# Kernel tuning notes

Hardware: AMD Instinct MI355X
Metric: run time of the kernel (lower is better)

Reference implementation:

```python
import jax, jax.numpy as jnp
import numpy as np
import math

B, T, F_ = 4, 1024, 1024
TO_DIM, FROM_DIM, LATENT, H = 1024, 1024, 1024, 16
HEAD_DIM = LATENT // H

def _linear_params(key, in_dim, out_dim):
    kw, kb = jax.random.split(key)
    bound = 1.0 / math.sqrt(in_dim)
    W = jax.random.uniform(kw, (out_dim, in_dim), minval=-bound, maxval=bound, dtype=jnp.float32)
    b = jax.random.uniform(kb, (out_dim,), minval=-bound, maxval=bound, dtype=jnp.float32)
    return W, b

def setup_inputs() -> dict:
    key = jax.random.key(0)
    ks = jax.random.split(key, 7)
    X_to = jax.random.normal(ks[0], (B, T, TO_DIM), dtype=jnp.float32)
    X_from = jax.random.normal(ks[1], (B, F_, FROM_DIM), dtype=jnp.float32)
    mask_from = jax.random.randint(ks[2], (B, T, F_), 0, 2, dtype=jnp.int32)
    Wq, bq = _linear_params(ks[3], TO_DIM, LATENT)
    Wk, bk = _linear_params(ks[4], FROM_DIM, LATENT)
    Wv, bv = _linear_params(ks[5], FROM_DIM, LATENT)
    Wo, bo = _linear_params(ks[6], LATENT, TO_DIM)
    return {"X_to": X_to, "X_from": X_from, "mask_from": mask_from,
            "Wq": Wq, "bq": bq, "Wk": Wk, "bk": bk, "Wv": Wv, "bv": bv, "Wo": Wo, "bo": bo}

def _split_heads(x):
    # [b, t, (h k)] -> [b, h, t, k]
    b, t, _ = x.shape
    return x.reshape(b, t, H, HEAD_DIM).transpose(0, 2, 1, 3)

def reference(X_to, X_from, mask_from, Wq, bq, Wk, bk, Wv, bv, Wo, bo):
    Q = _split_heads(X_to @ Wq.T + bq)
    # NOTE: source swaps names — K comes from v_linear, V from k_linear. Reproduced literally.
    K = _split_heads(X_from @ Wv.T + bv)
    V = _split_heads(X_from @ Wk.T + bk)
    attn = jnp.einsum('bhtk,bhfk->bhtf', Q, K) / math.sqrt(HEAD_DIM)
    attn = jnp.where(mask_from[:, None, :, :] == 0, jnp.float32(-10000.0), attn)
    attn = jax.nn.softmax(attn, axis=-1)
    out = jnp.einsum('bhtf,bhfk->bhtk', attn, V)  # [b,h,t,k]
    out = out.transpose(0, 2, 1, 3).reshape(X_to.shape[0], X_to.shape[1], LATENT)
    return out @ Wo.T + bo
```

## Files before the change

### kernel.cpp

```cpp
#include <hip/hip_runtime.h>
#include <hip/hip_bf16.h>
#include <math.h>

#define BB 4
#define TT 1024
#define FF 1024
#define DIM 1024
#define NH 16
#define HD 64
#define MROWS (BB * TT)
#define FB (FF / 64)

typedef __attribute__((ext_vector_type(8))) short short8;
typedef __attribute__((ext_vector_type(4))) short short4v;
typedef __attribute__((ext_vector_type(4))) float f32x4;
typedef __hip_bfloat16 bf16;

__device__ __forceinline__ void async_copy16(const void* g, void* l) {
    __builtin_amdgcn_global_load_lds((const __attribute__((address_space(1))) void*)g,
                                     (__attribute__((address_space(3))) void*)l,
                                     16, 0, 0);
}

struct ConvArgs {
    const float* src[6];
    bf16* dst[6];
    int nvec[6];
    int blk_end[6];
    const int* mask;
    unsigned long long* Mb;
};

__global__ __launch_bounds__(256) void convert_pack(ConvArgs a) {
    int bx = blockIdx.x;
    if (bx >= a.blk_end[5]) {
        const int lane = threadIdx.x & 63;
        const int waveId = (bx - a.blk_end[5]) * 4 + (threadIdx.x >> 6);
#pragma unroll
        for (int it = 0; it < 16; ++it) {
            int c = waveId * 16 + it;
            int v = a.mask[(size_t)c * 64 + lane];
            unsigned long long bits = __ballot(v != 0);
            if (lane == 0) a.Mb[c] = bits;
        }
        return;
    }
    int seg = 0;
#pragma unroll
    for (int k = 0; k < 5; ++k) if (bx >= a.blk_end[k]) seg = k + 1;
    int b0 = seg ? a.blk_end[seg - 1] : 0;
    int idx = (bx - b0) * 256 + threadIdx.x;
    if (idx >= a.nvec[seg]) return;
    float4 v = ((const float4*)a.src[seg])[idx];
    union { bf16 t[4]; ushort4 u; } o;
    o.t[0] = __float2bfloat16(v.x);
    o.t[1] = __float2bfloat16(v.y);
    o.t[2] = __float2bfloat16(v.z);
    o.t[3] = __float2bfloat16(v.w);
    *(ushort4*)(a.dst[seg] + 4 * (size_t)idx) = o.u;
}

#define BK 64

struct QkvArgs {
    const bf16* A[3]; const bf16* W[3]; const float* bias[3]; bf16* C[3];
    int N[3]; int biasRow[3];
};

__global__ __launch_bounds__(256) void gemm_qkv(QkvArgs q) {
    __shared__ bf16 smem[128 * 132];
    bf16* As = smem;
    bf16* Bs = smem + 128 * BK;

    const int op = blockIdx.z;
    const bf16* A = q.A[op];
    const bf16* W = q.W[op];
    const float* bias = q.bias[op];
    bf16* C = q.C[op];
    const int N = q.N[op];
    const int brow = q.biasRow[op];

    const int lin = blockIdx.x + 8 * blockIdx.y;
    const int xcd = lin & 7;
    const int t   = lin >> 3;
    int m0, n0;
    if (brow) {
        m0 = (((t & 7) + xcd) & 7) * 128;
        n0 = (xcd * 4 + (t >> 3)) * 128;
    } else {
        m0 = (xcd * 4 + (t >> 3)) * 128;
        n0 = (((t & 7) + xcd) & 7) * 128;
    }

    const int tid  = threadIdx.x;
    const int lane = tid & 63;
    const int wave = tid >> 6;
    const int quad = lane >> 4;
    const int l16  = lane & 15;
    const int wm = wave & 1;
    const int wn = wave >> 1;
    const int wbase = tid & ~63;

    f32x4 acc[4][4] = {};

    for (int k0 = 0; k0 < DIM; k0 += BK) {
#pragma unroll
        for (int j = 0; j < 4; ++j) {
            int slot = j * 256 + tid;
            int r = slot >> 3;
            int g = (slot & 7) ^ (r & 7);
            async_copy16(A + (size_t)(m0 + r) * DIM + k0 + g * 8,
                         As + (size_t)(j * 256 + wbase) * 8);
            async_copy16(W + (size_t)(n0 + r) * DIM + k0 + g * 8,
                         Bs + (size_t)(j * 256 + wbase) * 8);
        }
        __syncthreads();

#pragma unroll
        for (int kk = 0; kk < 2; ++kk) {
            short8 a[4], b[4];
#pragma unroll
            for (int mi = 0; mi < 4; ++mi) {
                int r = wm * 64 + mi * 16 + l16;
                int p = (kk * 4 + quad) ^ (r & 7);
                a[mi] = *(const short8*)(As + r * BK + p * 8);
            }
#pragma unroll
            for (int ni = 0; ni < 4; ++ni) {
                int r = wn * 64 + ni * 16 + l16;
                int p = (kk * 4 + quad) ^ (r & 7);
                b[ni] = *(const short8*)(Bs + r * BK + p * 8);
            }
#pragma unroll
            for (int mi = 0; mi < 4; ++mi)
#pragma unroll
                for (int ni = 0; ni < 4; ++ni)
                    acc[mi][ni] = __builtin_amdgcn_mfma_f32_16x16x32_bf16(
                        a[mi], b[ni], acc[mi][ni], 0, 0, 0);
        }
        __syncthreads();
    }

    bf16* Cs = smem;
#pragma unroll
    for (int ni = 0; ni < 4; ++ni) {
        const int nl = wn * 64 + ni * 16 + l16;
        float bcol = brow ? 0.0f : bias[n0 + nl];
#pragma unroll
        for (int mi = 0; mi < 4; ++mi)
#pragma unroll
            for (int i = 0; i < 4; ++i) {
                const int ml = wm * 64 + mi * 16 + quad * 4 + i;
                float v = acc[mi][ni][i] + (brow ? bias[m0 + ml] : bcol);
                Cs[ml * 132 + nl] = __float2bfloat16(v);
            }
    }
    __syncthreads();
#pragma unroll
    for (int j = 0; j < 8; ++j) {
        int slot = j * 256 + tid;
        int rr = slot >> 4, cc = slot & 15;
        short8 v = *(const short8*)(Cs + rr * 132 + cc * 8);
        *(short8*)(C + (size_t)(m0 + rr) * N + n0 + cc * 8) = v;
    }
}

__global__ __launch_bounds__(256) void gemm_o(
    const bf16* __restrict__ A, const bf16* __restrict__ W,
    const float* __restrict__ bias, float* __restrict__ C)
{
    __shared__ float smemf[128 * 66];
    bf16* As = (bf16*)smemf;
    bf16* Bs = As + 128 * BK;

    const int lin = blockIdx.x + 16 * blockIdx.y;
    const int xcd = lin & 7;
    const int t   = lin >> 3;
    const int m0 = (xcd * 4 + (t >> 4)) * 128;
    const int n0 = (((t & 15) + 2 * xcd) & 15) * 64;

    const int tid  = threadIdx.x;
    const int lane = tid & 63;
    const int wave = tid >> 6;
    const int quad = lane >> 4;
    const int l16  = lane & 15;
    const int wm = wave & 1;
    const int wn = wave >> 1;
    const int wbase = tid & ~63;

    f32x4 acc[4][2] = {};

    for (int k0 = 0; k0 < DIM; k0 += BK) {
#pragma unroll
        for (int j = 0; j < 4; ++j) {
            int slot = j * 256 + tid;
            int r = slot >> 3;
            int g = (slot & 7) ^ (r & 7);
            async_copy16(A + (size_t)(m0 + r) * DIM + k0 + g * 8,
                         As + (size_t)(j * 256 + wbase) * 8);
        }
#pragma unroll
        for (int j = 0; j < 2; ++j) {
            int slot = j * 256 + tid;
            int r = slot >> 3;
            int g = (slot & 7) ^ (r & 7);
            async_copy16(W + (size_t)(n0 + r) * DIM + k0 + g * 8,
                         Bs + (size_t)(j * 256 + wbase) * 8);
        }
        __syncthreads();

#pragma unroll
        for (int kk = 0; kk < 2; ++kk) {
            short8 a[4], b[2];
#pragma unroll
            for (int mi = 0; mi < 4; ++mi) {
                int r = wm * 64 + mi * 16 + l16;
                int p = (kk * 4 + quad) ^ (r & 7);
                a[mi] = *(const short8*)(As + r * BK + p * 8);
            }
#pragma unroll
            for (int ni = 0; ni < 2; ++ni) {
                int r = wn * 32 + ni * 16 + l16;
                int p = (kk * 4 + quad) ^ (r & 7);
                b[ni] = *(const short8*)(Bs + r * BK + p * 8);
            }
#pragma unroll
            for (int mi = 0; mi < 4; ++mi)
#pragma unroll
                for (int ni = 0; ni < 2; ++ni)
                    acc[mi][ni] = __builtin_amdgcn_mfma_f32_16x16x32_bf16(
                        a[mi], b[ni], acc[mi][ni], 0, 0, 0);
        }
        __syncthreads();
    }

    float* Cs = smemf;
#pragma unroll
    for (int ni = 0; ni < 2; ++ni) {
        const int nl = wn * 32 + ni * 16 + l16;
        const float bcol = bias[n0 + nl];
#pragma unroll
        for (int mi = 0; mi < 4; ++mi)
#pragma unroll
            for (int i = 0; i < 4; ++i) {
                const int ml = wm * 64 + mi * 16 + quad * 4 + i;
                Cs[ml * 66 + nl] = acc[mi][ni][i] + bcol;
            }
    }
    __syncthreads();
#pragma unroll
    for (int j = 0; j < 8; ++j) {
        int slot = j * 256 + tid;
        int rr = slot >> 4, cc = slot & 15;
        float4 v = *(const float4*)(Cs + rr * 66 + cc * 4);
        *(float4*)(C + (size_t)(m0 + rr) * DIM + n0 + cc * 4) = v;
    }
}

__global__ __launch_bounds__(256, 4) void attn_kernel(
    const bf16* Qg, const bf16* __restrict__ Kg, const bf16* __restrict__ Vtg,
    const unsigned long long* __restrict__ Mbits, bf16* Og)
{
    __shared__ bf16 Ks[128 * 64];
    __shared__ bf16 Vts[64 * 128];
    __shared__ bf16 Pt[64 * 136];
    __shared__ float ls[64];

    const int tid  = threadIdx.x;
    const int lane = tid & 63;
    const int wave = tid >> 6;
    const int quad = lane >> 4;
    const int l16  = lane & 15;

    const int lin = blockIdx.x + 16 * (blockIdx.y + 16 * blockIdx.z);
    const int xcd = lin & 7;
    const int t   = lin >> 3;
    const int bh  = xcd * 8 + (t >> 4);
    const int b   = bh >> 4;
    const int h   = bh & 15;
    const int t0  = (t & 15) * 64;

    const size_t qrow0 = (size_t)b * TT + t0;
    const size_t krow0 = (size_t)b * FF;
    const int wbase = tid & ~63;
    const int myrow = wave * 16 + l16;

    const bf16* qptr = Qg + (qrow0 + myrow) * DIM + h * HD;
    short8 qb0 = *(const short8*)(qptr + quad * 8);
    short8 qb1 = *(const short8*)(qptr + 32 + quad * 8);

    const unsigned long long* mrow = Mbits + (qrow0 + myrow) * FB;
    unsigned long long w0 = mrow[0];
    unsigned long long w1 = mrow[1];

    float lsum = 0.f;
    f32x4 oacc[4] = {};

#pragma unroll 1
    for (int it = 0; it < 8; ++it) {
        const int f0 = it * 128;
#pragma unroll
        for (int j = 0; j < 4; ++j) {
            int slot = j * 256 + tid;
            int rk = slot >> 3;
            int gk = (slot & 7) ^ (rk & 7);
            async_copy16(Kg + (krow0 + f0 + rk) * DIM + h * HD + gk * 8,
                         Ks + (size_t)(j * 256 + wbase) * 8);
            int rv = slot >> 4;
            int gv = (slot & 15) ^ (rv & 15);
            async_copy16(Vtg + (size_t)(h * HD + rv) * MROWS + b * FF + f0 + gv * 8,
                         Vts + (size_t)(j * 256 + wbase) * 8);
        }
        unsigned long long nw0 = 0, nw1 = 0;
        if (it < 7) { nw0 = mrow[2 * it + 2]; nw1 = mrow[2 * it + 3]; }
        __syncthreads();

        f32x4 sacc[8];
#pragma unroll
        for (int ft = 0; ft < 8; ++ft) {
            int r = ft * 16 + l16;
            short8 ka0 = *(const short8*)(Ks + r * 64 + ((quad       ^ (r & 7)) * 8));
            short8 ka1 = *(const short8*)(Ks + r * 64 + (((quad + 4) ^ (r & 7)) * 8));
            f32x4 s = {};
            s = __builtin_amdgcn_mfma_f32_16x16x32_bf16(ka0, qb0, s, 0, 0, 0);
            s = __builtin_amdgcn_mfma_f32_16x16x32_bf16(ka1, qb1, s, 0, 0, 0);
            sacc[ft] = s;
        }

#pragma unroll
        for (int ft = 0; ft < 8; ++ft) {
            const unsigned long long word = (ft < 4) ? w0 : w1;
            const unsigned bits4 =
                (unsigned)(word >> ((ft & 3) * 16 + quad * 4)) & 0xFu;
            union { short4v v; short s[4]; } pk;
            float psum = 0.f;
#pragma unroll
            for (int i = 0; i < 4; ++i) {
                float p = (bits4 >> i) & 1u ? __expf(sacc[ft][i] * 0.125f) : 0.f;
                psum += p;
                pk.s[i] = (short)__bfloat16_as_ushort(__float2bfloat16(p));
            }
            lsum += psum;
            *(short4v*)(Pt + myrow * 136 + ft * 16 + quad * 4) = pk.v;
        }
        w0 = nw0; w1 = nw1;

        short8 pa[4];
#pragma unroll
        for (int kf = 0; kf < 4; ++kf)
            pa[kf] = *(const short8*)(Pt + myrow * 136 + kf * 32 + quad * 8);
#pragma unroll
        for (int nt = 0; nt < 4; ++nt) {
            int rd = nt * 16 + l16;
#pragma unroll
            for (int kf = 0; kf < 4; ++kf) {
                int g = (kf * 4 + quad) ^ (rd & 15);
                short8 vb = *(const short8*)(Vts + rd * 128 + g * 8);
                oacc[nt] = __builtin_amdgcn_mfma_f32_16x16x32_bf16(pa[kf], vb, oacc[nt], 0, 0, 0);
            }
        }
        __syncthreads();
    }

    lsum += __shfl_xor(lsum, 16);
    lsum += __shfl_xor(lsum, 32);
    if (quad == 0) ls[myrow] = lsum;

#pragma unroll
    for (int i = 0; i < 4; ++i) {
        float inv = 1.0f / ls[wave * 16 + quad * 4 + i];
        const int prow = wave * 16 + quad * 4 + i;
#pragma unroll
        for (int nt = 0; nt < 4; ++nt)
            Pt[prow * 136 + nt * 16 + l16] = __float2bfloat16(oacc[nt][i] * inv);
    }
    __syncthreads();
#pragma unroll
    for (int j = 0; j < 2; ++j) {
        int s = j * 256 + tid;
        int rr = s >> 3, off = (s & 7) * 8;
        short8 v = *(const short8*)(Pt + rr * 136 + off);
        *(short8*)(Og + (qrow0 + rr) * DIM + h * HD + off) = v;
    }
}

extern "C" void kernel_launch(void* const* d_in, const int* in_sizes, int n_in,
                              void* d_out, int out_size, void* d_ws, size_t ws_size,
                              hipStream_t stream) {
    const float* X_to   = (const float*)d_in[0];
    const float* X_from = (const float*)d_in[1];
    const int*   mask   = (const int*)  d_in[2];
    const float* Wq     = (const float*)d_in[3];
    const float* bq     = (const float*)d_in[4];
    const float* Wk     = (const float*)d_in[5];
    const float* bk     = (const float*)d_in[6];
    const float* Wv     = (const float*)d_in[7];
    const float* bv     = (const float*)d_in[8];
    const float* Wo     = (const float*)d_in[9];
    const float* bo     = (const float*)d_in[10];
    float* out = (float*)d_out;

    char* ws = (char*)d_ws;
    bf16* Xt16 = (bf16*)(ws);
    bf16* Xf16 = (bf16*)(ws + (8u  << 20));
    bf16* Wq16 = (bf16*)(ws + (16u << 20));
    bf16* Wv16 = (bf16*)(ws + (18u << 20));
    bf16* Wk16 = (bf16*)(ws + (20u << 20));
    bf16* Wo16 = (bf16*)(ws + (22u << 20));
    bf16* Q16  = (bf16*)(ws + (24u << 20));
    bf16* K16  = (bf16*)(ws + (32u << 20));
    bf16* Vt16 = (bf16*)(ws + (40u << 20));
    unsigned long long* Mb = (unsigned long long*)(ws + (48u << 20));

    ConvArgs ca;
    ca.src[0] = X_to;   ca.dst[0] = Xt16; ca.nvec[0] = MROWS * DIM / 4;
    ca.src[1] = X_from; ca.dst[1] = Xf16; ca.nvec[1] = MROWS * DIM / 4;
    ca.src[2] = Wq;     ca.dst[2] = Wq16; ca.nvec[2] = DIM * DIM / 4;
    ca.src[3] = Wv;     ca.dst[3] = Wv16; ca.nvec[3] = DIM * DIM / 4;
    ca.src[4] = Wk;     ca.dst[4] = Wk16; ca.nvec[4] = DIM * DIM / 4;
    ca.src[5] = Wo;     ca.dst[5] = Wo16; ca.nvec[5] = DIM * DIM / 4;
    int cum = 0;
    for (int k = 0; k < 6; ++k) { cum += ca.nvec[k] / 256; ca.blk_end[k] = cum; }
    ca.mask = mask; ca.Mb = Mb;
    convert_pack<<<cum + 1024, 256, 0, stream>>>(ca);

    QkvArgs qa;
    qa.A[0] = Xt16; qa.W[0] = Wq16; qa.bias[0] = bq; qa.C[0] = Q16;
    qa.N[0] = DIM; qa.biasRow[0] = 0;
    qa.A[1] = Xf16; qa.W[1] = Wv16; qa.bias[1] = bv; qa.C[1] = K16;
    qa.N[1] = DIM; qa.biasRow[1] = 0;
    qa.A[2] = Wk16; qa.W[2] = Xf16; qa.bias[2] = bk; qa.C[2] = Vt16;
    qa.N[2] = MROWS; qa.biasRow[2] = 1;
    gemm_qkv<<<dim3(8, 32, 3), 256, 0, stream>>>(qa);

    attn_kernel<<<dim3(TT / 64, NH, BB), 256, 0, stream>>>(
        Q16, K16, Vt16, Mb, Q16);

    gemm_o<<<dim3(DIM / 64, MROWS / 128), 256, 0, stream>>>(Q16, Wo16, bo, out);
}
```

Baseline: 229.7 us.

## Halve GEMM K-tile to 32 and stage epilogue in two halves

Both projection GEMMs now use a K-tile of 32 instead of 64 and write the epilogue through shared memory in two 64-row halves. Together these shrink the shared-memory footprint so more blocks can be resident per CU. The XCD-aware block swizzle is also dropped in favour of plain blockIdx tile mapping. In exchange the main loop runs twice as many iterations, each with a pair of barriers and less MFMA work to cover load latency, and L2 locality across XCDs may get worse.

```diff
diff --git a/kernel.cpp b/kernel.cpp
--- a/kernel.cpp
+++ b/kernel.cpp
@@ -60,7 +60,7 @@
     *(ushort4*)(a.dst[seg] + 4 * (size_t)idx) = o.u;
 }
 
-#define BK 64
+#define BKq 32
 
 struct QkvArgs {
     const bf16* A[3]; const bf16* W[3]; const float* bias[3]; bf16* C[3];
@@ -68,9 +68,10 @@
 };
 
 __global__ __launch_bounds__(256) void gemm_qkv(QkvArgs q) {
-    __shared__ bf16 smem[128 * 132];
-    bf16* As = smem;
-    bf16* Bs = smem + 128 * BK;
+    __shared__ char smem[64 * 136 * 2];
+    bf16* As = (bf16*)smem;
+    bf16* Bs = As + 128 * BKq;
+    bf16* Cs = (bf16*)smem;
 
     const int op = blockIdx.z;
     const bf16* A = q.A[op];
@@ -80,17 +81,9 @@
     const int N = q.N[op];
     const int brow = q.biasRow[op];
 
-    const int lin = blockIdx.x + 8 * blockIdx.y;
-    const int xcd = lin & 7;
-    const int t   = lin >> 3;
     int m0, n0;
-    if (brow) {
-        m0 = (((t & 7) + xcd) & 7) * 128;
-        n0 = (xcd * 4 + (t >> 3)) * 128;
-    } else {
-        m0 = (xcd * 4 + (t >> 3)) * 128;
-        n0 = (((t & 7) + xcd) & 7) * 128;
-    }
+    if (brow) { m0 = blockIdx.x * 128; n0 = blockIdx.y * 128; }
+    else      { n0 = blockIdx.x * 128; m0 = blockIdx.y * 128; }
 
     const int tid  = threadIdx.x;
     const int lane = tid & 63;
@@ -103,12 +96,12 @@
 
     f32x4 acc[4][4] = {};
 
-    for (int k0 = 0; k0 < DIM; k0 += BK) {
-#pragma unroll
-        for (int j = 0; j < 4; ++j) {
+    for (int k0 = 0; k0 < DIM; k0 += BKq) {
+#pragma unroll
+        for (int j = 0; j < 2; ++j) {
             int slot = j * 256 + tid;
-            int r = slot >> 3;
-            int g = (slot & 7) ^ (r & 7);
+            int r = slot >> 2;
+            int g = (slot & 3) ^ (r & 3);
             async_copy16(A + (size_t)(m0 + r) * DIM + k0 + g * 8,
                          As + (size_t)(j * 256 + wbase) * 8);
             async_copy16(W + (size_t)(n0 + r) * DIM + k0 + g * 8,
@@ -116,52 +109,53 @@
         }
         __syncthreads();
 
-#pragma unroll
-        for (int kk = 0; kk < 2; ++kk) {
-            short8 a[4], b[4];
-#pragma unroll
-            for (int mi = 0; mi < 4; ++mi) {
-                int r = wm * 64 + mi * 16 + l16;
-                int p = (kk * 4 + quad) ^ (r & 7);
-                a[mi] = *(const short8*)(As + r * BK + p * 8);
+        short8 a[4], b[4];
+#pragma unroll
+        for (int mi = 0; mi < 4; ++mi) {
+            int r = wm * 64 + mi * 16 + l16;
+            a[mi] = *(const short8*)(As + r * BKq + ((quad ^ (r & 3)) * 8));
+        }
+#pragma unroll
+        for (int ni = 0; ni < 4; ++ni) {
+            int r = wn * 64 + ni * 16 + l16;
+            b[ni] = *(const short8*)(Bs + r * BKq + ((quad ^ (r & 3)) * 8));
+        }
+#pragma unroll
+        for (int mi = 0; mi < 4; ++mi)
+#pragma unroll
+            for (int ni = 0; ni < 4; ++ni)
+                acc[mi][ni] = __builtin_amdgcn_mfma_f32_16x16x32_bf16(
+                    a[mi], b[ni], acc[mi][ni], 0, 0, 0);
+        __syncthreads();
+    }
+
+#pragma unroll
+    for (int half = 0; half < 2; ++half) {
+        if (wm == half) {
+#pragma unroll
+            for (int ni = 0; ni < 4; ++ni) {
+                const int nl = wn * 64 + ni * 16 + l16;
+                float bcol = brow ? 0.0f : bias[n0 + nl];
+#pragma unroll
+                for (int mi = 0; mi < 4; ++mi)
+#pragma unroll
+                    for (int i = 0; i < 4; ++i) {
+                        const int mloc = mi * 16 + quad * 4 + i;
+                        float v = acc[mi][ni][i] +
+                                  (brow ? bias[m0 + half * 64 + mloc] : bcol);
+                        Cs[mloc * 136 + nl] = __float2bfloat16(v);
+                    }
             }
-#pragma unroll
-            for (int ni = 0; ni < 4; ++ni) {
-                int r = wn * 64 + ni * 16 + l16;
-                int p = (kk * 4 + quad) ^ (r & 7);
-                b[ni] = *(const short8*)(Bs + r * BK + p * 8);
-            }
-#pragma unroll
-            for (int mi = 0; mi < 4; ++mi)
-#pragma unroll
-                for (int ni = 0; ni < 4; ++ni)
-                    acc[mi][ni] = __builtin_amdgcn_mfma_f32_16x16x32_bf16(
-                        a[mi], b[ni], acc[mi][ni], 0, 0, 0);
-        }
-        __syncthreads();
-    }
-
-    bf16* Cs = smem;
-#pragma unroll
-    for (int ni = 0; ni < 4; ++ni) {
-        const int nl = wn * 64 + ni * 16 + l16;
-        float bcol = brow ? 0.0f : bias[n0 + nl];
-#pragma unroll
-        for (int mi = 0; mi < 4; ++mi)
-#pragma unroll
-            for (int i = 0; i < 4; ++i) {
-                const int ml = wm * 64 + mi * 16 + quad * 4 + i;
-                float v = acc[mi][ni][i] + (brow ? bias[m0 + ml] : bcol);
-                Cs[ml * 132 + nl] = __float2bfloat16(v);
-            }
-    }
-    __syncthreads();
-#pragma unroll
-    for (int j = 0; j < 8; ++j) {
-        int slot = j * 256 + tid;
-        int rr = slot >> 4, cc = slot & 15;
-        short8 v = *(const short8*)(Cs + rr * 132 + cc * 8);
-        *(short8*)(C + (size_t)(m0 + rr) * N + n0 + cc * 8) = v;
+        }
+        __syncthreads();
+#pragma unroll
+        for (int j = 0; j < 4; ++j) {
+            int slot = j * 256 + tid;
+            int rr = slot >> 4, cc = slot & 15;
+            short8 v = *(const short8*)(Cs + rr * 136 + cc * 8);
+            *(short8*)(C + (size_t)(m0 + half * 64 + rr) * N + n0 + cc * 8) = v;
+        }
+        __syncthreads();
     }
 }
 
@@ -169,16 +163,13 @@
     const bf16* __restrict__ A, const bf16* __restrict__ W,
     const float* __restrict__ bias, float* __restrict__ C)
 {
-    __shared__ float smemf[128 * 66];
-    bf16* As = (bf16*)smemf;
-    bf16* Bs = As + 128 * BK;
-
-    const int lin = blockIdx.x + 16 * blockIdx.y;
-    const int xcd = lin & 7;
-    const int t   = lin >> 3;
-    const int m0 = (xcd * 4 + (t >> 4)) * 128;
-    const int n0 = (((t & 15) + 2 * xcd) & 15) * 64;
-
+    __shared__ char smem[64 * 68 * 4];
+    bf16* As = (bf16*)smem;
+    bf16* Bs = As + 128 * BKq;
+    float* Cs = (float*)smem;
+
+    const int n0 = blockIdx.x * 64;
+    const int m0 = blockIdx.y * 128;
     const int tid  = threadIdx.x;
     const int lane = tid & 63;
     const int wave = tid >> 6;
@@ -190,70 +181,68 @@
 
     f32x4 acc[4][2] = {};
 
-    for (int k0 = 0; k0 < DIM; k0 += BK) {
+    for (int k0 = 0; k0 < DIM; k0 += BKq) {
+#pragma unroll
+        for (int j = 0; j < 2; ++j) {
+            int slot = j * 256 + tid;
+            int r = slot >> 2;
+            int g = (slot & 3) ^ (r & 3);
+            async_copy16(A + (size_t)(m0 + r) * DIM + k0 + g * 8,
+                         As + (size_t)(j * 256 + wbase) * 8);
+        }
+        {
+            int r = tid >> 2;
+            int g = (tid & 3) ^ (r & 3);
+            async_copy16(W + (size_t)(n0 + r) * DIM + k0 + g * 8,
+                         Bs + (size_t)wbase * 8);
+        }
+        __syncthreads();
+
+        short8 a[4], b[2];
+#pragma unroll
+        for (int mi = 0; mi < 4; ++mi) {
+            int r = wm * 64 + mi * 16 + l16;
+            a[mi] = *(const short8*)(As + r * BKq + ((quad ^ (r & 3)) * 8));
+        }
+#pragma unroll
+        for (int ni = 0; ni < 2; ++ni) {
+            int r = wn * 32 + ni * 16 + l16;
+            b[ni] = *(const short8*)(Bs + r * BKq + ((quad ^ (r & 3)) * 8));
+        }
+#pragma unroll
+        for (int mi = 0; mi < 4; ++mi)
+#pragma unroll
+            for (int ni = 0; ni < 2; ++ni)
+                acc[mi][ni] = __builtin_amdgcn_mfma_f32_16x16x32_bf16(
+                    a[mi], b[ni], acc[mi][ni], 0, 0, 0);
+        __syncthreads();
+    }
+
+#pragma unroll
+    for (int half = 0; half < 2; ++half) {
+        if (wm == half) {
+#pragma unroll
+            for (int ni = 0; ni < 2; ++ni) {
+                const int nl = wn * 32 + ni * 16 + l16;
+                const float bcol = bias[n0 + nl];
+#pragma unroll
+                for (int mi = 0; mi < 4; ++mi)
+#pragma unroll
+                    for (int i = 0; i < 4; ++i) {
+                        const int mloc = mi * 16 + quad * 4 + i;
+                        Cs[mloc * 68 + nl] = acc[mi][ni][i] + bcol;
+                    }
+            }
+        }
+        __syncthreads();
 #pragma unroll
         for (int j = 0; j < 4; ++j) {
             int slot = j * 256 + tid;
-            int r = slot >> 3;
-            int g = (slot & 7) ^ (r & 7);
-            async_copy16(A + (size_t)(m0 + r) * DIM + k0 + g * 8,
-                         As + (size_t)(j * 256 + wbase) * 8);
-        }
-#pragma unroll
-        for (int j = 0; j < 2; ++j) {
-            int slot = j * 256 + tid;
-            int r = slot >> 3;
-            int g = (slot & 7) ^ (r & 7);
-            async_copy16(W + (size_t)(n0 + r) * DIM + k0 + g * 8,
-                         Bs + (size_t)(j * 256 + wbase) * 8);
-        }
-        __syncthreads();
-
-#pragma unroll
-        for (int kk = 0; kk < 2; ++kk) {
-            short8 a[4], b[2];
-#pragma unroll
-            for (int mi = 0; mi < 4; ++mi) {
-                int r = wm * 64 + mi * 16 + l16;
-                int p = (kk * 4 + quad) ^ (r & 7);
-                a[mi] = *(const short8*)(As + r * BK + p * 8);
-            }
-#pragma unroll
-            for (int ni = 0; ni < 2; ++ni) {
-                int r = wn * 32 + ni * 16 + l16;
-                int p = (kk * 4 + quad) ^ (r & 7);
-                b[ni] = *(const short8*)(Bs + r * BK + p * 8);
-            }
-#pragma unroll
-            for (int mi = 0; mi < 4; ++mi)
-#pragma unroll
-                for (int ni = 0; ni < 2; ++ni)
-                    acc[mi][ni] = __builtin_amdgcn_mfma_f32_16x16x32_bf16(
-                        a[mi], b[ni], acc[mi][ni], 0, 0, 0);
-        }
-        __syncthreads();
-    }
-
-    float* Cs = smemf;
-#pragma unroll
-    for (int ni = 0; ni < 2; ++ni) {
-        const int nl = wn * 32 + ni * 16 + l16;
-        const float bcol = bias[n0 + nl];
-#pragma unroll
-        for (int mi = 0; mi < 4; ++mi)
-#pragma unroll
-            for (int i = 0; i < 4; ++i) {
-                const int ml = wm * 64 + mi * 16 + quad * 4 + i;
-                Cs[ml * 66 + nl] = acc[mi][ni][i] + bcol;
-            }
-    }
-    __syncthreads();
-#pragma unroll
-    for (int j = 0; j < 8; ++j) {
-        int slot = j * 256 + tid;
-        int rr = slot >> 4, cc = slot & 15;
-        float4 v = *(const float4*)(Cs + rr * 66 + cc * 4);
-        *(float4*)(C + (size_t)(m0 + rr) * DIM + n0 + cc * 4) = v;
+            int rr = slot >> 4, cc = slot & 15;
+            float4 v = *(const float4*)(Cs + rr * 68 + cc * 4);
+            *(float4*)(C + (size_t)(m0 + half * 64 + rr) * DIM + n0 + cc * 4) = v;
+        }
+        __syncthreads();
     }
 }
 
```

Measured after the change: 230.6 us. No clear change (+0.4%).
